# Optimization experiments

Hardware: AMD Instinct MI355X
Metric: run time of the kernel (lower is better)

## Reference

```python
import jax, jax.numpy as jnp
import numpy as np

N_OBJ, N_EVT, N_EDGE, N_MAIN = 50000, 100000, 500000, 25000
OBJ_DIM, EVT_DIM = 256, 256


def setup_inputs() -> dict:
    key = jax.random.key(0)
    ks = jax.random.split(key, 12)
    s = 1.0 / np.sqrt(OBJ_DIM)
    return {
        "object_X": jax.random.normal(ks[0], (N_OBJ, OBJ_DIM), jnp.float32),
        "event_X": jax.random.normal(ks[1], (N_EVT, EVT_DIM), jnp.float32),
        "lc_obj_idx": jax.random.randint(ks[2], (N_EDGE,), 0, N_OBJ),
        "lc_evt_idx": jax.random.randint(ks[3], (N_EDGE,), 0, N_EVT),
        "main_idx": jax.random.randint(ks[4], (N_MAIN,), 0, N_OBJ),
        # lifecycle_proj: Linear(event_dim, obj_dim)
        "W_proj": jax.random.uniform(ks[5], (OBJ_DIM, EVT_DIM), jnp.float32, -s, s),
        "b_proj": jax.random.uniform(ks[6], (OBJ_DIM,), jnp.float32, -s, s),
        # GRUCell(obj_dim, obj_dim): weight_ih/hh are [3*H, H]
        "W_ih": jax.random.uniform(ks[7], (3 * OBJ_DIM, OBJ_DIM), jnp.float32, -s, s),
        "b_ih": jax.random.uniform(ks[8], (3 * OBJ_DIM,), jnp.float32, -s, s),
        "W_hh": jax.random.uniform(ks[9], (3 * OBJ_DIM, OBJ_DIM), jnp.float32, -s, s),
        "b_hh": jax.random.uniform(ks[10], (3 * OBJ_DIM,), jnp.float32, -s, s),
    }


def reference(object_X, event_X, lc_obj_idx, lc_evt_idx, main_idx,
              W_proj, b_proj, W_ih, b_ih, W_hh, b_hh):
    n_obj = object_X.shape[0]
    # gather event feats, linear + ReLU  -> [E, obj_dim]
    proj = jax.nn.relu(event_X[lc_evt_idx] @ W_proj.T + b_proj)
    # scatter_mean over target objects (empty slots -> 0, like torch_scatter)
    sums = jax.ops.segment_sum(proj, lc_obj_idx, num_segments=n_obj)
    cnt = jax.ops.segment_sum(jnp.ones((lc_obj_idx.shape[0],), proj.dtype),
                              lc_obj_idx, num_segments=n_obj)
    profile = sums / jnp.maximum(cnt, 1.0)[:, None]  # [N_obj, obj_dim]
    # GRUCell(profile, object_X)
    gi = profile @ W_ih.T + b_ih   # [N_obj, 3H]
    gh = object_X @ W_hh.T + b_hh  # [N_obj, 3H]
    i_r, i_z, i_n = jnp.split(gi, 3, axis=-1)
    h_r, h_z, h_n = jnp.split(gh, 3, axis=-1)
    r = jax.nn.sigmoid(i_r + h_r)
    z = jax.nn.sigmoid(i_z + h_z)
    n = jnp.tanh(i_n + r * h_n)
    updated = (1.0 - z) * n + z * object_X
    # masked blend: only main objects take updated values
    mask = jnp.zeros((n_obj, 1), object_X.dtype).at[main_idx].set(1.0)
    return mask * updated + (1.0 - mask) * object_X
```

## Files before the change

### kernel.cpp

```cpp
#include <hip/hip_runtime.h>

typedef unsigned short u16;
typedef __attribute__((ext_vector_type(8))) short bf16x8;
typedef __attribute__((ext_vector_type(4))) float f32x4;

struct __align__(8) u16x4_t { u16 x, y, z, w; };

__device__ __forceinline__ float b2f(u16 b) {
  union { unsigned u; float f; } v; v.u = ((unsigned)b) << 16; return v.f;
}
__device__ __forceinline__ u16 f2b(float f) {
  union { float f; unsigned u; } v; v.f = f;
  unsigned r = v.u + 0x7fffu + ((v.u >> 16) & 1u);
  return (u16)(r >> 16);
}

__global__ void set_mask_append(const int* __restrict__ main_idx, int* __restrict__ mask,
                                int* __restrict__ mlist, int* __restrict__ cpos,
                                int* __restrict__ mcount, int n) {
  int t = blockIdx.x * 256 + threadIdx.x;
  if (t >= n) return;
  int o = main_idx[t];
  if (atomicCAS(&mask[o], 0, 1) == 0) {
    int i = atomicAdd(mcount, 1);
    mlist[i] = o;
    cpos[o] = i;
  }
}

__global__ void build_rrows(const int* __restrict__ mlist, const int* __restrict__ mcount,
                            int* __restrict__ rrows, int Mpad) {
  int t = blockIdx.x * 256 + threadIdx.x;
  if (t >= Mpad) return;
  int mc = *mcount;
  rrows[t] = (t < mc) ? mlist[t] : 0;
}

__global__ void cvt_f32_bf16(const float* __restrict__ src, u16* __restrict__ dst, int n4) {
  int t = blockIdx.x * 256 + threadIdx.x;
  if (t >= n4) return;
  float4 v = ((const float4*)src)[t];
  u16x4_t o;
  o.x = f2b(v.x); o.y = f2b(v.y); o.z = f2b(v.z); o.w = f2b(v.w);
  ((u16x4_t*)dst)[t] = o;
}

__global__ void count_edges(const int* __restrict__ obj_idx, const int* __restrict__ mask,
                            int* __restrict__ deg, int n) {
  int e = blockIdx.x * 256 + threadIdx.x;
  if (e >= n) return;
  int o = obj_idx[e];
  if (mask[o]) atomicAdd(&deg[o], 1);
}

__global__ void scan_block(const int* __restrict__ deg, int* __restrict__ offs,
                           int* __restrict__ bsum, int n) {
  __shared__ int tmp[256];
  int t = threadIdx.x;
  int i = blockIdx.x * 256 + t;
  int v = (i < n) ? deg[i] : 0;
  tmp[t] = v;
  __syncthreads();
  for (int off = 1; off < 256; off <<= 1) {
    int x = (t >= off) ? tmp[t - off] : 0;
    __syncthreads();
    tmp[t] += x;
    __syncthreads();
  }
  if (i < n) offs[i] = tmp[t] - v;
  if (t == 255) bsum[blockIdx.x] = tmp[255];
}

__global__ void scan_tops(int* __restrict__ bsum, int nb) {
  __shared__ int tmp[256];
  int t = threadIdx.x;
  int v = (t < nb) ? bsum[t] : 0;
  tmp[t] = v;
  __syncthreads();
  for (int off = 1; off < 256; off <<= 1) {
    int x = (t >= off) ? tmp[t - off] : 0;
    __syncthreads();
    tmp[t] += x;
    __syncthreads();
  }
  if (t < nb) bsum[t] = tmp[t] - v;
}

__global__ void scan_add(int* __restrict__ offs, const int* __restrict__ bsum, int n) {
  int i = blockIdx.x * 256 + threadIdx.x;
  if (i < n) offs[i] += bsum[blockIdx.x];
}

__global__ void fill_edges(const int* __restrict__ obj_idx, const int* __restrict__ evt_idx,
                           const int* __restrict__ mask, const int* __restrict__ offs,
                           int* __restrict__ cursor, int* __restrict__ elist, int n) {
  int e = blockIdx.x * 256 + threadIdx.x;
  if (e >= n) return;
  int o = obj_idx[e];
  if (!mask[o]) return;
  int pos = atomicAdd(&cursor[o], 1);
  elist[offs[o] + pos] = evt_idx[e];
}

__global__ __launch_bounds__(256)
void accum_prof(const u16* __restrict__ P, const int* __restrict__ elist,
                const int* __restrict__ offs, const int* __restrict__ deg,
                const int* __restrict__ mlist, const int* __restrict__ mcount,
                u16* __restrict__ prof, int Mpad) {
  const int wave = threadIdx.x >> 6;
  const int lane = threadIdx.x & 63;
  const int i = blockIdx.x * 4 + wave;
  if (i >= Mpad) return;
  const int mc = *mcount;
  float a0 = 0.f, a1 = 0.f, a2 = 0.f, a3 = 0.f;
  int d = 0;
  if (i < mc) {
    const int o = mlist[i];
    const int off = offs[o];
    d = deg[o];
    int j = 0;
    for (; j + 1 < d; j += 2) {
      int e0 = elist[off + j], e1 = elist[off + j + 1];
      u16x4_t p0 = *(const u16x4_t*)(P + (size_t)e0 * 256 + lane * 4);
      u16x4_t p1 = *(const u16x4_t*)(P + (size_t)e1 * 256 + lane * 4);
      a0 += b2f(p0.x) + b2f(p1.x);
      a1 += b2f(p0.y) + b2f(p1.y);
      a2 += b2f(p0.z) + b2f(p1.z);
      a3 += b2f(p0.w) + b2f(p1.w);
    }
    if (j < d) {
      int e0 = elist[off + j];
      u16x4_t p0 = *(const u16x4_t*)(P + (size_t)e0 * 256 + lane * 4);
      a0 += b2f(p0.x); a1 += b2f(p0.y); a2 += b2f(p0.z); a3 += b2f(p0.w);
    }
  }
  float s = 1.f / fmaxf((float)d, 1.f);
  u16x4_t ov;
  ov.x = f2b(a0 * s); ov.y = f2b(a1 * s); ov.z = f2b(a2 * s); ov.w = f2b(a3 * s);
  *(u16x4_t*)(prof + (size_t)i * 256 + lane * 4) = ov;
}

template<int RELU, int GATHER>
__global__ __launch_bounds__(256, 2)
void gemm_bt_bf16(const u16* __restrict__ A, const u16* __restrict__ B,
                  const float* __restrict__ bias, u16* __restrict__ C,
                  const int* __restrict__ ridx, int M, int N, int K) {
  __shared__ u16 lA[128 * 64];
  __shared__ u16 lB[128 * 64];
  const int tid  = threadIdx.x;
  const int lane = tid & 63;
  const int wave = tid >> 6;
  const int m0 = blockIdx.x * 128;
  const int n0 = blockIdx.y * 128;

  f32x4 acc[4][4] = {};

  const int mR = (wave & 1) * 64;
  const int nC = (wave >> 1) * 64;

  for (int kt = 0; kt < K; kt += 64) {
    __syncthreads();
#pragma unroll
    for (int s = 0; s < 4; ++s) {
      int slot = s * 256 + tid;
      int row  = slot >> 3;
      int kk   = (slot & 7) * 8;
      int ar;
      if (GATHER) {
        ar = ridx[m0 + row];
      } else {
        ar = m0 + row; ar = (ar < M) ? ar : (M - 1);
      }
      const u16* gA = A + (size_t)ar * K + (kt + kk);
      __builtin_amdgcn_global_load_lds(
          (const __attribute__((address_space(1))) void*)gA,
          (__attribute__((address_space(3))) void*)(lA + s * 2048 + wave * 512),
          16, 0, 0);
      const u16* gB = B + (size_t)(n0 + row) * K + (kt + kk);
      __builtin_amdgcn_global_load_lds(
          (const __attribute__((address_space(1))) void*)gB,
          (__attribute__((address_space(3))) void*)(lB + s * 2048 + wave * 512),
          16, 0, 0);
    }
    __syncthreads();

#pragma unroll
    for (int ks = 0; ks < 2; ++ks) {
      const int kb = ks * 32 + (lane >> 4) * 8;
      bf16x8 af[4], bfr[4];
#pragma unroll
      for (int i = 0; i < 4; ++i) {
        af[i]  = *(const bf16x8*)(lA + (mR + i * 16 + (lane & 15)) * 64 + kb);
        bfr[i] = *(const bf16x8*)(lB + (nC + i * 16 + (lane & 15)) * 64 + kb);
      }
#pragma unroll
      for (int i = 0; i < 4; ++i)
#pragma unroll
        for (int j = 0; j < 4; ++j)
          acc[i][j] = __builtin_amdgcn_mfma_f32_16x16x32_bf16(af[i], bfr[j], acc[i][j], 0, 0, 0);
    }
  }

  const int crow = (lane >> 4) * 4;
  const int ccol = lane & 15;
#pragma unroll
  for (int i = 0; i < 4; ++i) {
#pragma unroll
    for (int j = 0; j < 4; ++j) {
      int col = n0 + nC + j * 16 + ccol;
      float bv = bias[col];
#pragma unroll
      for (int q = 0; q < 4; ++q) {
        int row = m0 + mR + i * 16 + crow + q;
        if (row < M) {
          float v = acc[i][j][q] + bv;
          if (RELU) v = fmaxf(v, 0.f);
          C[(size_t)row * N + col] = f2b(v);
        }
      }
    }
  }
}

__global__ __launch_bounds__(256)
void gate_out(const u16* __restrict__ gi, const u16* __restrict__ gh,
              const float* __restrict__ objX, const int* __restrict__ mask,
              const int* __restrict__ cpos, float* __restrict__ out, int nObj) {
  const int row = blockIdx.x;
  const int d = threadIdx.x;
  const size_t o256 = (size_t)row * 256 + d;
  float x = objX[o256];
  float res = x;
  if (mask[row]) {
    const size_t c768 = (size_t)cpos[row] * 768 + d;
    float ir = b2f(gi[c768]), iz = b2f(gi[c768 + 256]), inn = b2f(gi[c768 + 512]);
    float hr = b2f(gh[c768]), hz = b2f(gh[c768 + 256]), hn = b2f(gh[c768 + 512]);
    float r = 1.f / (1.f + __expf(-(ir + hr)));
    float z = 1.f / (1.f + __expf(-(iz + hz)));
    float a = inn + r * hn;
    float n = 1.f - 2.f / (__expf(2.f * a) + 1.f);
    res = (1.f - z) * n + z * x;
  }
  out[o256] = res;
}


extern "C" void kernel_launch(void* const* d_in, const int* in_sizes, int n_in,
                              void* d_out, int out_size, void* d_ws, size_t ws_size,
                              hipStream_t stream) {
  const float* objX   = (const float*)d_in[0];
  const float* evtX   = (const float*)d_in[1];
  const int* obj_idx  = (const int*)d_in[2];
  const int* evt_idx  = (const int*)d_in[3];
  const int* main_idx = (const int*)d_in[4];
  const float* Wp = (const float*)d_in[5];
  const float* bp = (const float*)d_in[6];
  const float* Wi = (const float*)d_in[7];
  const float* bi = (const float*)d_in[8];
  const float* Wh = (const float*)d_in[9];
  const float* bh = (const float*)d_in[10];

  const int nObj  = in_sizes[0] / 256;
  const int nEvt  = in_sizes[1] / 256;
  const int nEdge = in_sizes[2];
  const int nMain = in_sizes[4];
  const int Mpad  = ((nMain + 127) / 128) * 128;

  char* ws = (char*)d_ws;
  u16*   evtb  = (u16*)(ws + 0);
  u16*   P     = (u16*)(ws + 51200000);
  u16*   objb  = (u16*)(ws + 102400000);
  u16*   prof  = (u16*)(ws + 128000000);
  u16*   wpb   = (u16*)(ws + 140845056);
  u16*   wib   = (u16*)(ws + 140976128);
  u16*   whb   = (u16*)(ws + 141369344);
  int*   deg   = (int*)(ws + 141762560);
  int*   offs  = (int*)(ws + 141962560);
  int*   cursor= (int*)(ws + 142162560);
  int*   mask  = (int*)(ws + 142362560);
  int*   cpos  = (int*)(ws + 142562560);
  int*   mlist = (int*)(ws + 142762560);
  int*   rrows = (int*)(ws + 142862912);
  int*   bsum  = (int*)(ws + 142963264);
  int*   mcount= (int*)(ws + 142964288);
  int*   elist = (int*)(ws + 142964352);
  u16*   gi    = (u16*)(ws + 0);
  u16*   gh    = (u16*)(ws + 51200000);
  float* out   = (float*)d_out;

  hipMemsetAsync(ws + 141762560, 0, 1201792, stream);

  set_mask_append<<<(nMain + 255) / 256, 256, 0, stream>>>(main_idx, mask, mlist, cpos, mcount, nMain);

  cvt_f32_bf16<<<(in_sizes[1] / 4 + 255) / 256, 256, 0, stream>>>(evtX, evtb, in_sizes[1] / 4);
  cvt_f32_bf16<<<(in_sizes[0] / 4 + 255) / 256, 256, 0, stream>>>(objX, objb, in_sizes[0] / 4);
  cvt_f32_bf16<<<(65536 / 4 + 255) / 256, 256, 0, stream>>>(Wp, wpb, 65536 / 4);
  cvt_f32_bf16<<<(196608 / 4 + 255) / 256, 256, 0, stream>>>(Wi, wib, 196608 / 4);
  cvt_f32_bf16<<<(196608 / 4 + 255) / 256, 256, 0, stream>>>(Wh, whb, 196608 / 4);

  gemm_bt_bf16<1, 0><<<dim3((nEvt + 127) / 128, 2), 256, 0, stream>>>(
      evtb, wpb, bp, P, nullptr, nEvt, 256, 256);

  count_edges<<<(nEdge + 255) / 256, 256, 0, stream>>>(obj_idx, mask, deg, nEdge);
  scan_block<<<(nObj + 255) / 256, 256, 0, stream>>>(deg, offs, bsum, nObj);
  scan_tops<<<1, 256, 0, stream>>>(bsum, (nObj + 255) / 256);
  scan_add<<<(nObj + 255) / 256, 256, 0, stream>>>(offs, bsum, nObj);
  fill_edges<<<(nEdge + 255) / 256, 256, 0, stream>>>(obj_idx, evt_idx, mask, offs, cursor, elist, nEdge);

  accum_prof<<<(Mpad + 3) / 4, 256, 0, stream>>>(P, elist, offs, deg, mlist, mcount, prof, Mpad);

  build_rrows<<<(Mpad + 255) / 256, 256, 0, stream>>>(mlist, mcount, rrows, Mpad);

  gemm_bt_bf16<0, 0><<<dim3(Mpad / 128, 6), 256, 0, stream>>>(
      prof, wib, bi, gi, nullptr, Mpad, 768, 256);
  gemm_bt_bf16<0, 1><<<dim3(Mpad / 128, 6), 256, 0, stream>>>(
      objb, whb, bh, gh, rrows, Mpad, 768, 256);

  gate_out<<<nObj, 256, 0, stream>>>(gi, gh, objX, mask, cpos, out, nObj);
}
```

Measured before the change: 418.7 us.

## Fuse fp32-to-bf16 conversion into GEMM A-tile loads and merge small kernels

```diff
diff --git a/kernel.cpp b/kernel.cpp
--- a/kernel.cpp
+++ b/kernel.cpp
@@ -28,21 +28,17 @@
   }
 }
 
-__global__ void build_rrows(const int* __restrict__ mlist, const int* __restrict__ mcount,
-                            int* __restrict__ rrows, int Mpad) {
+__global__ void cvt_weights(const float* __restrict__ Wp, const float* __restrict__ Wi,
+                            const float* __restrict__ Wh, u16* __restrict__ wb) {
   int t = blockIdx.x * 256 + threadIdx.x;
-  if (t >= Mpad) return;
-  int mc = *mcount;
-  rrows[t] = (t < mc) ? mlist[t] : 0;
-}
-
-__global__ void cvt_f32_bf16(const float* __restrict__ src, u16* __restrict__ dst, int n4) {
-  int t = blockIdx.x * 256 + threadIdx.x;
-  if (t >= n4) return;
-  float4 v = ((const float4*)src)[t];
-  u16x4_t o;
-  o.x = f2b(v.x); o.y = f2b(v.y); o.z = f2b(v.z); o.w = f2b(v.w);
-  ((u16x4_t*)dst)[t] = o;
+  const float* src; int o;
+  if (t < 16384)      { src = Wp; o = t; }
+  else if (t < 65536) { src = Wi; o = t - 16384; }
+  else                { src = Wh; o = t - 65536; }
+  float4 v = ((const float4*)src)[o];
+  u16x4_t q;
+  q.x = f2b(v.x); q.y = f2b(v.y); q.z = f2b(v.z); q.w = f2b(v.w);
+  ((u16x4_t*)wb)[t] = q;
 }
 
 __global__ void count_edges(const int* __restrict__ obj_idx, const int* __restrict__ mask,
@@ -86,9 +82,15 @@
   if (t < nb) bsum[t] = tmp[t] - v;
 }
 
-__global__ void scan_add(int* __restrict__ offs, const int* __restrict__ bsum, int n) {
+__global__ void scan_add_rrows(int* __restrict__ offs, const int* __restrict__ bsum,
+                               const int* __restrict__ mlist, const int* __restrict__ mcount,
+                               int* __restrict__ rrows, int n, int Mpad) {
   int i = blockIdx.x * 256 + threadIdx.x;
   if (i < n) offs[i] += bsum[blockIdx.x];
+  if (i < Mpad) {
+    int mc = *mcount;
+    rrows[i] = (i < mc) ? mlist[i] : 0;
+  }
 }
 
 __global__ void fill_edges(const int* __restrict__ obj_idx, const int* __restrict__ evt_idx,
@@ -140,11 +142,12 @@
   *(u16x4_t*)(prof + (size_t)i * 256 + lane * 4) = ov;
 }
 
-template<int RELU, int GATHER>
+template<int RELU, int GATHER, int CVT>
 __global__ __launch_bounds__(256, 2)
-void gemm_bt_bf16(const u16* __restrict__ A, const u16* __restrict__ B,
-                  const float* __restrict__ bias, u16* __restrict__ C,
-                  const int* __restrict__ ridx, int M, int N, int K) {
+void gemm_bt(const u16* __restrict__ Ab, const float* __restrict__ Af,
+             const u16* __restrict__ B, const float* __restrict__ bias,
+             u16* __restrict__ C, const int* __restrict__ ridx,
+             int M, int N, int K) {
   __shared__ u16 lA[128 * 64];
   __shared__ u16 lB[128 * 64];
   const int tid  = threadIdx.x;
@@ -154,33 +157,57 @@
   const int n0 = blockIdx.y * 128;
 
   f32x4 acc[4][4] = {};
-
   const int mR = (wave & 1) * 64;
   const int nC = (wave >> 1) * 64;
 
+  int arow[4], brow[4], kkv[4];
+#pragma unroll
+  for (int s = 0; s < 4; ++s) {
+    int slot = s * 256 + tid;
+    int row  = slot >> 3;
+    kkv[s]   = (slot & 7) * 8;
+    int ar;
+    if (GATHER) ar = ridx[m0 + row];
+    else { ar = m0 + row; ar = (ar < M) ? ar : (M - 1); }
+    arow[s] = ar;
+    brow[s] = n0 + row;
+  }
+
   for (int kt = 0; kt < K; kt += 64) {
     __syncthreads();
+    float4 va[4][2];
 #pragma unroll
     for (int s = 0; s < 4; ++s) {
       int slot = s * 256 + tid;
-      int row  = slot >> 3;
-      int kk   = (slot & 7) * 8;
-      int ar;
-      if (GATHER) {
-        ar = ridx[m0 + row];
-      } else {
-        ar = m0 + row; ar = (ar < M) ? ar : (M - 1);
-      }
-      const u16* gA = A + (size_t)ar * K + (kt + kk);
-      __builtin_amdgcn_global_load_lds(
-          (const __attribute__((address_space(1))) void*)gA,
-          (__attribute__((address_space(3))) void*)(lA + s * 2048 + wave * 512),
-          16, 0, 0);
-      const u16* gB = B + (size_t)(n0 + row) * K + (kt + kk);
+      const u16* gB = B + (size_t)brow[s] * K + (kt + kkv[s]);
       __builtin_amdgcn_global_load_lds(
           (const __attribute__((address_space(1))) void*)gB,
           (__attribute__((address_space(3))) void*)(lB + s * 2048 + wave * 512),
           16, 0, 0);
+      if (CVT) {
+        const float* gA = Af + (size_t)arow[s] * K + (kt + kkv[s]);
+        va[s][0] = *(const float4*)gA;
+        va[s][1] = *(const float4*)(gA + 4);
+      } else {
+        const u16* gA = Ab + (size_t)arow[s] * K + (kt + kkv[s]);
+        __builtin_amdgcn_global_load_lds(
+            (const __attribute__((address_space(1))) void*)gA,
+            (__attribute__((address_space(3))) void*)(lA + s * 2048 + wave * 512),
+            16, 0, 0);
+      }
+      (void)slot;
+    }
+    if (CVT) {
+#pragma unroll
+      for (int s = 0; s < 4; ++s) {
+        int slot = s * 256 + tid;
+        bf16x8 w;
+        w[0] = (short)f2b(va[s][0].x); w[1] = (short)f2b(va[s][0].y);
+        w[2] = (short)f2b(va[s][0].z); w[3] = (short)f2b(va[s][0].w);
+        w[4] = (short)f2b(va[s][1].x); w[5] = (short)f2b(va[s][1].y);
+        w[6] = (short)f2b(va[s][1].z); w[7] = (short)f2b(va[s][1].w);
+        *(bf16x8*)(lA + slot * 8) = w;
+      }
     }
     __syncthreads();
 
@@ -267,54 +294,46 @@
   const int Mpad  = ((nMain + 127) / 128) * 128;
 
   char* ws = (char*)d_ws;
-  u16*   evtb  = (u16*)(ws + 0);
-  u16*   P     = (u16*)(ws + 51200000);
-  u16*   objb  = (u16*)(ws + 102400000);
-  u16*   prof  = (u16*)(ws + 128000000);
-  u16*   wpb   = (u16*)(ws + 140845056);
-  u16*   wib   = (u16*)(ws + 140976128);
-  u16*   whb   = (u16*)(ws + 141369344);
-  int*   deg   = (int*)(ws + 141762560);
-  int*   offs  = (int*)(ws + 141962560);
-  int*   cursor= (int*)(ws + 142162560);
-  int*   mask  = (int*)(ws + 142362560);
-  int*   cpos  = (int*)(ws + 142562560);
-  int*   mlist = (int*)(ws + 142762560);
-  int*   rrows = (int*)(ws + 142862912);
-  int*   bsum  = (int*)(ws + 142963264);
-  int*   mcount= (int*)(ws + 142964288);
-  int*   elist = (int*)(ws + 142964352);
+  u16*   P     = (u16*)(ws + 0);
   u16*   gi    = (u16*)(ws + 0);
   u16*   gh    = (u16*)(ws + 51200000);
+  u16*   prof  = (u16*)(ws + 89735168);
+  u16*   wb    = (u16*)(ws + 102580224);
+  u16*   wpb   = wb;
+  u16*   wib   = wb + 65536;
+  u16*   whb   = wb + 262144;
+  int*   deg   = (int*)(ws + 103497728);
+  int*   offs  = (int*)(ws + 103697728);
+  int*   cursor= (int*)(ws + 103897728);
+  int*   mask  = (int*)(ws + 104097728);
+  int*   cpos  = (int*)(ws + 104297728);
+  int*   mlist = (int*)(ws + 104497728);
+  int*   rrows = (int*)(ws + 104598080);
+  int*   bsum  = (int*)(ws + 104698432);
+  int*   mcount= (int*)(ws + 104699456);
+  int*   elist = (int*)(ws + 104699520);
   float* out   = (float*)d_out;
 
-  hipMemsetAsync(ws + 141762560, 0, 1201792, stream);
+  hipMemsetAsync(ws + 103497728, 0, 1201792, stream);
 
   set_mask_append<<<(nMain + 255) / 256, 256, 0, stream>>>(main_idx, mask, mlist, cpos, mcount, nMain);
-
-  cvt_f32_bf16<<<(in_sizes[1] / 4 + 255) / 256, 256, 0, stream>>>(evtX, evtb, in_sizes[1] / 4);
-  cvt_f32_bf16<<<(in_sizes[0] / 4 + 255) / 256, 256, 0, stream>>>(objX, objb, in_sizes[0] / 4);
-  cvt_f32_bf16<<<(65536 / 4 + 255) / 256, 256, 0, stream>>>(Wp, wpb, 65536 / 4);
-  cvt_f32_bf16<<<(196608 / 4 + 255) / 256, 256, 0, stream>>>(Wi, wib, 196608 / 4);
-  cvt_f32_bf16<<<(196608 / 4 + 255) / 256, 256, 0, stream>>>(Wh, whb, 196608 / 4);
-
-  gemm_bt_bf16<1, 0><<<dim3((nEvt + 127) / 128, 2), 256, 0, stream>>>(
-      evtb, wpb, bp, P, nullptr, nEvt, 256, 256);
+  cvt_weights<<<448, 256, 0, stream>>>(Wp, Wi, Wh, wb);
+
+  gemm_bt<1, 0, 1><<<dim3((nEvt + 127) / 128, 2), 256, 0, stream>>>(
+      nullptr, evtX, wpb, bp, P, nullptr, nEvt, 256, 256);
 
   count_edges<<<(nEdge + 255) / 256, 256, 0, stream>>>(obj_idx, mask, deg, nEdge);
   scan_block<<<(nObj + 255) / 256, 256, 0, stream>>>(deg, offs, bsum, nObj);
   scan_tops<<<1, 256, 0, stream>>>(bsum, (nObj + 255) / 256);
-  scan_add<<<(nObj + 255) / 256, 256, 0, stream>>>(offs, bsum, nObj);
+  scan_add_rrows<<<(nObj + 255) / 256, 256, 0, stream>>>(offs, bsum, mlist, mcount, rrows, nObj, Mpad);
   fill_edges<<<(nEdge + 255) / 256, 256, 0, stream>>>(obj_idx, evt_idx, mask, offs, cursor, elist, nEdge);
 
   accum_prof<<<(Mpad + 3) / 4, 256, 0, stream>>>(P, elist, offs, deg, mlist, mcount, prof, Mpad);
 
-  build_rrows<<<(Mpad + 255) / 256, 256, 0, stream>>>(mlist, mcount, rrows, Mpad);
-
-  gemm_bt_bf16<0, 0><<<dim3(Mpad / 128, 6), 256, 0, stream>>>(
-      prof, wib, bi, gi, nullptr, Mpad, 768, 256);
-  gemm_bt_bf16<0, 1><<<dim3(Mpad / 128, 6), 256, 0, stream>>>(
-      objb, whb, bh, gh, rrows, Mpad, 768, 256);
+  gemm_bt<0, 0, 0><<<dim3(Mpad / 128, 6), 256, 0, stream>>>(
+      prof, nullptr, wib, bi, gi, nullptr, Mpad, 768, 256);
+  gemm_bt<0, 1, 1><<<dim3(Mpad / 128, 6), 256, 0, stream>>>(
+      nullptr, objX, whb, bh, gh, rrows, Mpad, 768, 256);
 
   gate_out<<<nObj, 256, 0, stream>>>(gi, gh, objX, mask, cpos, out, nObj);
 }
```

After: 422.8 us. Within noise of the previous version (+1.0%).
